# Kernel tuning notes

Hardware: AMD Instinct MI355X
Metric: run time of the kernel (lower is better)

## Reference

```python
import jax, jax.numpy as jnp
import numpy as np

B, L, H, Z = 16, 2048, 1024, 512
NEG = -1e9


def setup_inputs() -> dict:
    key = jax.random.key(0)
    ks = jax.random.split(key, 7)
    return {
        "encoder_rnn_hidden_states": jax.random.normal(ks[0], (B, L, H), jnp.float32),
        "encoder_final_hidden_state": jax.random.normal(ks[1], (B, H), jnp.float32),
        "latent_z_seq": jax.random.normal(ks[2], (B, L, Z), jnp.float32),
        "mask": jax.random.randint(ks[3], (B, L), 0, 2, jnp.int32),
        "weight_q": jax.random.normal(ks[4], (H, H), jnp.float32),
        "weight_k": jax.random.normal(ks[5], (H, H), jnp.float32),
        "weight_v": jax.random.normal(ks[6], (Z, Z), jnp.float32),
    }


def reference(encoder_rnn_hidden_states, encoder_final_hidden_state, latent_z_seq,
              mask, weight_q, weight_k, weight_v):
    temperature = jnp.asarray(weight_q.shape[0] ** 0.5, encoder_rnn_hidden_states.dtype)
    # final hidden state is repeated along src_len, so project once: [B,H]
    k = encoder_final_hidden_state @ weight_k              # [B,H]
    q = encoder_rnn_hidden_states @ weight_q               # [B,L,H]
    v = latent_z_seq @ weight_v                            # [B,L,Z]
    # alignment[b,i,j] = q[b,i] . k[b]  (identical across j, per original repeat)
    alignment = jnp.einsum('bih,bh->bi', q, k) / temperature  # [B,L]
    alignment = jnp.broadcast_to(alignment[:, :, None], (q.shape[0], q.shape[1], q.shape[1]))
    # mask[:, :, None] tiled over last dim; fill -1e9 where mask == 0
    alignment = jnp.where(mask[:, :, None] == 0, NEG, alignment)
    # softmax over the QUERY axis (dim=-2), not the usual key axis
    attn = jax.nn.softmax(alignment, axis=-2)              # [B,L,L]
    output = jnp.einsum('bij,bjz->biz', attn, v)           # [B,L,Z]
    return output, attn
```

## Files before the change

kernel.cpp:

```cpp
#include <hip/hip_runtime.h>

#define BB 16
#define LL 2048
#define HH 1024
#define ZZ 512
#define NEGV -1e9f

__global__ __launch_bounds__(256) void k_proj_k(const float* __restrict__ efhs,
                                                const float* __restrict__ Wk,
                                                float* __restrict__ kbuf) {
    int blk = blockIdx.x;
    int b   = blk >> 5;
    int hpc = (blk >> 3) & 3;
    int hc  = blk & 7;
    int hp  = hpc * 256 + threadIdx.x;
    const float* e  = efhs + b * HH + hc * 128;
    const float* wk = Wk + (size_t)(hc * 128) * HH + hp;
    float acc = 0.f;
#pragma unroll 4
    for (int h = 0; h < 128; ++h)
        acc += e[h] * wk[(size_t)h * HH];
    atomicAdd(&kbuf[b * HH + hp], acc);
}

__global__ __launch_bounds__(256) void k_proj_kq(const float* __restrict__ Wq,
                                                 const float* __restrict__ kbuf,
                                                 float* __restrict__ kq) {
    int h = blockIdx.x >> 2;
    int b = ((blockIdx.x & 3) << 2) + (threadIdx.x >> 6);
    int lane = threadIdx.x & 63;
    const float4* wrow = (const float4*)(Wq + (size_t)h * HH);
    const float4* kb   = (const float4*)(kbuf + b * HH);
    float acc = 0.f;
#pragma unroll
    for (int u = 0; u < 4; ++u) {
        float4 wv = wrow[u * 64 + lane];
        float4 kv = kb[u * 64 + lane];
        acc += wv.x * kv.x + wv.y * kv.y + wv.z * kv.z + wv.w * kv.w;
    }
    for (int off = 32; off > 0; off >>= 1) acc += __shfl_down(acc, off);
    if (lane == 0) kq[b * HH + h] = acc;
}

__global__ __launch_bounds__(256) void k_scores_zsum(const float* __restrict__ erhs,
                                                     const float* __restrict__ kq,
                                                     const int* __restrict__ mask,
                                                     const float* __restrict__ zseq,
                                                     float* __restrict__ sbuf,
                                                     float* __restrict__ zsum) {
    if (blockIdx.x < 8192) {
        int row = blockIdx.x * 4 + (threadIdx.x >> 6);
        int lane = threadIdx.x & 63;
        int b = row >> 11;
        const float4* e  = (const float4*)(erhs + (size_t)row * HH);
        const float4* kb = (const float4*)(kq + b * HH);
        float acc = 0.f;
#pragma unroll
        for (int u = 0; u < 4; ++u) {
            float4 ev = e[u * 64 + lane];
            float4 kv = kb[u * 64 + lane];
            acc += ev.x * kv.x + ev.y * kv.y + ev.z * kv.z + ev.w * kv.w;
        }
        for (int off = 32; off > 0; off >>= 1) acc += __shfl_down(acc, off);
        if (lane == 0) {
            float v = acc * (1.0f / 32.0f);
            if (mask[row] == 0) v = NEGV;
            sbuf[row] = v;
        }
    } else {
        int blk = blockIdx.x - 8192;
        int b = blk >> 5, jc = blk & 31;
        int t = threadIdx.x;
        const float* p = zseq + ((size_t)(b * LL + jc * 64)) * ZZ;
        float a0 = 0.f, a1 = 0.f;
        for (int j = 0; j < 64; ++j) {
            const float* pj = p + (size_t)j * ZZ;
            a0 += pj[t];
            a1 += pj[t + 256];
        }
        atomicAdd(&zsum[b * ZZ + t], a0);
        atomicAdd(&zsum[b * ZZ + t + 256], a1);
    }
}

__global__ __launch_bounds__(256) void k_softmax_vsum(const float* __restrict__ sbuf,
                                                      const float* __restrict__ zsum,
                                                      const float* __restrict__ Wv,
                                                      float* __restrict__ wbuf,
                                                      float* __restrict__ Vs) {
    __shared__ float es[LL];
    __shared__ float red[16];
    if (blockIdx.x < 16) {
        int b = blockIdx.x, tid = threadIdx.x;
        int wave = tid >> 6, lane = tid & 63;
        const float* sb = sbuf + b * LL;
        float m = -3.4e38f;
        for (int i = tid; i < LL; i += 256) m = fmaxf(m, sb[i]);
        for (int off = 32; off > 0; off >>= 1) m = fmaxf(m, __shfl_down(m, off));
        if (lane == 0) red[wave] = m;
        __syncthreads();
        if (tid == 0) {
            float mm = red[0];
            for (int i = 1; i < 4; ++i) mm = fmaxf(mm, red[i]);
            red[0] = mm;
        }
        __syncthreads();
        m = red[0];
        float ssum = 0.f;
        for (int i = tid; i < LL; i += 256) {
            float e = __expf(sb[i] - m);
            es[i] = e;
            ssum += e;
        }
        for (int off = 32; off > 0; off >>= 1) ssum += __shfl_down(ssum, off);
        if (lane == 0) red[8 + wave] = ssum;
        __syncthreads();
        if (tid == 0) {
            float tt = 0.f;
            for (int i = 0; i < 4; ++i) tt += red[8 + i];
            red[8] = tt;
        }
        __syncthreads();
        float inv = 1.0f / red[8];
        for (int i = tid; i < LL; i += 256) wbuf[b * LL + i] = es[i] * inv;
    } else {
        int blk = blockIdx.x - 16;
        int b = blk >> 3, z0c = blk & 7;
        int t = threadIdx.x;
        const float* zs = zsum + b * ZZ + z0c * 64;
        const float* wv = Wv + (size_t)(z0c * 64) * ZZ;
        float a0 = 0.f, a1 = 0.f;
        for (int z0 = 0; z0 < 64; ++z0) {
            float zv = zs[z0];
            const float* wr = wv + (size_t)z0 * ZZ;
            a0 += zv * wr[t];
            a1 += zv * wr[t + 256];
        }
        atomicAdd(&Vs[b * ZZ + t], a0);
        atomicAdd(&Vs[b * ZZ + t + 256], a1);
    }
}

__global__ __launch_bounds__(256) void k_outattn(const float* __restrict__ wbuf,
                                                 const float* __restrict__ Vs,
                                                 float* __restrict__ out,
                                                 float* __restrict__ attn) {
    int row = blockIdx.x;
    int b = row >> 11;
    int t = threadIdx.x;
    float wv = wbuf[row];
    if (t < 128) {
        float4 v = ((const float4*)(Vs + b * ZZ))[t];
        ((float4*)(out + (size_t)row * ZZ))[t] =
            make_float4(wv * v.x, wv * v.y, wv * v.z, wv * v.w);
    }
    float4 pk = make_float4(wv, wv, wv, wv);
    float4* p = (float4*)attn + (size_t)row * 512;
    p[t]       = pk;
    p[t + 256] = pk;
}

extern "C" void kernel_launch(void* const* d_in, const int* in_sizes, int n_in,
                              void* d_out, int out_size, void* d_ws, size_t ws_size,
                              hipStream_t stream) {
    const float* erhs = (const float*)d_in[0];
    const float* efhs = (const float*)d_in[1];
    const float* zseq = (const float*)d_in[2];
    const int*   mask = (const int*)d_in[3];
    const float* Wq   = (const float*)d_in[4];
    const float* Wk   = (const float*)d_in[5];
    const float* Wv   = (const float*)d_in[6];
    float* out = (float*)d_out;

    float* ws   = (float*)d_ws;
    float* zsum = ws;
    float* kbuf = ws + 8192;
    float* Vs   = ws + 24576;
    float* sbuf = ws + 32768;
    float* wbuf = ws + 65536;
    float* kq   = ws + 98304;

    hipMemsetAsync(ws, 0, 32768 * sizeof(float), stream);
    k_proj_k      <<<  512, 256, 0, stream>>>(efhs, Wk, kbuf);
    k_proj_kq     <<< 4096, 256, 0, stream>>>(Wq, kbuf, kq);
    k_scores_zsum <<< 8704, 256, 0, stream>>>(erhs, kq, mask, zseq, sbuf, zsum);
    k_softmax_vsum<<<  144, 256, 0, stream>>>(sbuf, zsum, Wv, wbuf, Vs);
    k_outattn     <<<32768, 256, 0, stream>>>(wbuf, Vs, out,
                                              out + (size_t)BB * LL * ZZ);
}
```

Baseline: 503.4 us.

## Fuse all stages into one cooperative persistent kernel with grid syncs

Replaces the five separate launches with a single cooperative kernel of 1024 blocks that runs every stage (k projection, z sum, kq projection, V sum, scores, softmax, output/attn writes) separated by grid-wide syncs. It also reworks the per-stage work split so each block or wave handles several rows, which reuses loaded k/W vectors across rows and batches. The aim is to remove launch gaps and tail effects between small kernels. In exchange, a grid sync costs something, the softmax stage keeps only 16 blocks busy while the rest wait, and the final write stage uses fewer, larger blocks, which may lower write throughput.

```diff
diff --git a/kernel.cpp b/kernel.cpp
--- a/kernel.cpp
+++ b/kernel.cpp
@@ -1,76 +1,61 @@
 #include <hip/hip_runtime.h>
+#include <hip/hip_cooperative_groups.h>
+
+namespace cg = cooperative_groups;
 
 #define BB 16
 #define LL 2048
 #define HH 1024
 #define ZZ 512
 #define NEGV -1e9f
+#define GRID 1024
 
-__global__ __launch_bounds__(256) void k_proj_k(const float* __restrict__ efhs,
-                                                const float* __restrict__ Wk,
-                                                float* __restrict__ kbuf) {
-    int blk = blockIdx.x;
-    int b   = blk >> 5;
-    int hpc = (blk >> 3) & 3;
-    int hc  = blk & 7;
-    int hp  = hpc * 256 + threadIdx.x;
-    const float* e  = efhs + b * HH + hc * 128;
-    const float* wk = Wk + (size_t)(hc * 128) * HH + hp;
-    float acc = 0.f;
-#pragma unroll 4
-    for (int h = 0; h < 128; ++h)
-        acc += e[h] * wk[(size_t)h * HH];
-    atomicAdd(&kbuf[b * HH + hp], acc);
+__device__ __forceinline__ float dot4(float4 a, float4 b) {
+    return a.x * b.x + a.y * b.y + a.z * b.z + a.w * b.w;
 }
 
-__global__ __launch_bounds__(256) void k_proj_kq(const float* __restrict__ Wq,
-                                                 const float* __restrict__ kbuf,
-                                                 float* __restrict__ kq) {
-    int h = blockIdx.x >> 2;
-    int b = ((blockIdx.x & 3) << 2) + (threadIdx.x >> 6);
-    int lane = threadIdx.x & 63;
-    const float4* wrow = (const float4*)(Wq + (size_t)h * HH);
-    const float4* kb   = (const float4*)(kbuf + b * HH);
-    float acc = 0.f;
-#pragma unroll
-    for (int u = 0; u < 4; ++u) {
-        float4 wv = wrow[u * 64 + lane];
-        float4 kv = kb[u * 64 + lane];
-        acc += wv.x * kv.x + wv.y * kv.y + wv.z * kv.z + wv.w * kv.w;
-    }
-    for (int off = 32; off > 0; off >>= 1) acc += __shfl_down(acc, off);
-    if (lane == 0) kq[b * HH + h] = acc;
-}
+__global__ __launch_bounds__(256, 4) void k_fused(
+    const float* __restrict__ erhs, const float* __restrict__ efhs,
+    const float* __restrict__ zseq, const int* __restrict__ mask,
+    const float* __restrict__ Wq, const float* __restrict__ Wk,
+    const float* __restrict__ Wv, float* __restrict__ out,
+    float* __restrict__ attn, float* __restrict__ ws)
+{
+    float* zsum = ws;
+    float* kbuf = ws + 8192;
+    float* Vs   = ws + 24576;
+    float* sbuf = ws + 32768;
+    float* wbuf = ws + 65536;
+    float* kq   = ws + 98304;
 
-__global__ __launch_bounds__(256) void k_scores_zsum(const float* __restrict__ erhs,
-                                                     const float* __restrict__ kq,
-                                                     const int* __restrict__ mask,
-                                                     const float* __restrict__ zseq,
-                                                     float* __restrict__ sbuf,
-                                                     float* __restrict__ zsum) {
-    if (blockIdx.x < 8192) {
-        int row = blockIdx.x * 4 + (threadIdx.x >> 6);
-        int lane = threadIdx.x & 63;
-        int b = row >> 11;
-        const float4* e  = (const float4*)(erhs + (size_t)row * HH);
-        const float4* kb = (const float4*)(kq + b * HH);
-        float acc = 0.f;
-#pragma unroll
-        for (int u = 0; u < 4; ++u) {
-            float4 ev = e[u * 64 + lane];
-            float4 kv = kb[u * 64 + lane];
-            acc += ev.x * kv.x + ev.y * kv.y + ev.z * kv.z + ev.w * kv.w;
+    cg::grid_group grid = cg::this_grid();
+    const int beta = blockIdx.x;
+    const int t    = threadIdx.x;
+    const int wid  = t >> 6, lane = t & 63;
+
+    __shared__ float es[LL];
+    __shared__ float red[16];
+
+    if (beta < 64) {
+        int b = beta >> 2, hseg = beta & 3;
+        const float* e  = efhs + b * HH + hseg * 256;
+        const float* wk = Wk + (size_t)(hseg * 256) * HH;
+        float a0 = 0.f, a1 = 0.f, a2 = 0.f, a3 = 0.f;
+        for (int h = 0; h < 256; ++h) {
+            float ev = e[h];
+            const float* wr = wk + (size_t)h * HH;
+            a0 += ev * wr[t];
+            a1 += ev * wr[t + 256];
+            a2 += ev * wr[t + 512];
+            a3 += ev * wr[t + 768];
         }
-        for (int off = 32; off > 0; off >>= 1) acc += __shfl_down(acc, off);
-        if (lane == 0) {
-            float v = acc * (1.0f / 32.0f);
-            if (mask[row] == 0) v = NEGV;
-            sbuf[row] = v;
-        }
-    } else {
-        int blk = blockIdx.x - 8192;
+        atomicAdd(&kbuf[b * HH + t],       a0);
+        atomicAdd(&kbuf[b * HH + t + 256], a1);
+        atomicAdd(&kbuf[b * HH + t + 512], a2);
+        atomicAdd(&kbuf[b * HH + t + 768], a3);
+    } else if (beta < 576) {
+        int blk = beta - 64;
         int b = blk >> 5, jc = blk & 31;
-        int t = threadIdx.x;
         const float* p = zseq + ((size_t)(b * LL + jc * 64)) * ZZ;
         float a0 = 0.f, a1 = 0.f;
         for (int j = 0; j < 64; ++j) {
@@ -78,55 +63,26 @@
             a0 += pj[t];
             a1 += pj[t + 256];
         }
-        atomicAdd(&zsum[b * ZZ + t], a0);
+        atomicAdd(&zsum[b * ZZ + t],       a0);
         atomicAdd(&zsum[b * ZZ + t + 256], a1);
     }
-}
+    grid.sync();
 
-__global__ __launch_bounds__(256) void k_softmax_vsum(const float* __restrict__ sbuf,
-                                                      const float* __restrict__ zsum,
-                                                      const float* __restrict__ Wv,
-                                                      float* __restrict__ wbuf,
-                                                      float* __restrict__ Vs) {
-    __shared__ float es[LL];
-    __shared__ float red[16];
-    if (blockIdx.x < 16) {
-        int b = blockIdx.x, tid = threadIdx.x;
-        int wave = tid >> 6, lane = tid & 63;
-        const float* sb = sbuf + b * LL;
-        float m = -3.4e38f;
-        for (int i = tid; i < LL; i += 256) m = fmaxf(m, sb[i]);
-        for (int off = 32; off > 0; off >>= 1) m = fmaxf(m, __shfl_down(m, off));
-        if (lane == 0) red[wave] = m;
-        __syncthreads();
-        if (tid == 0) {
-            float mm = red[0];
-            for (int i = 1; i < 4; ++i) mm = fmaxf(mm, red[i]);
-            red[0] = mm;
+    if (beta < 256) {
+        int h = beta * 4 + wid;
+        const float4* wrow = (const float4*)(Wq + (size_t)h * HH);
+        float4 w0 = wrow[lane], w1 = wrow[64 + lane],
+               w2 = wrow[128 + lane], w3 = wrow[192 + lane];
+        for (int b = 0; b < BB; ++b) {
+            const float4* kb = (const float4*)(kbuf + b * HH);
+            float acc = dot4(w0, kb[lane]) + dot4(w1, kb[64 + lane])
+                      + dot4(w2, kb[128 + lane]) + dot4(w3, kb[192 + lane]);
+            for (int off = 32; off > 0; off >>= 1) acc += __shfl_down(acc, off);
+            if (lane == 0) kq[b * HH + h] = acc;
         }
-        __syncthreads();
-        m = red[0];
-        float ssum = 0.f;
-        for (int i = tid; i < LL; i += 256) {
-            float e = __expf(sb[i] - m);
-            es[i] = e;
-            ssum += e;
-        }
-        for (int off = 32; off > 0; off >>= 1) ssum += __shfl_down(ssum, off);
-        if (lane == 0) red[8 + wave] = ssum;
-        __syncthreads();
-        if (tid == 0) {
-            float tt = 0.f;
-            for (int i = 0; i < 4; ++i) tt += red[8 + i];
-            red[8] = tt;
-        }
-        __syncthreads();
-        float inv = 1.0f / red[8];
-        for (int i = tid; i < LL; i += 256) wbuf[b * LL + i] = es[i] * inv;
-    } else {
-        int blk = blockIdx.x - 16;
+    } else if (beta < 384) {
+        int blk = beta - 256;
         int b = blk >> 3, z0c = blk & 7;
-        int t = threadIdx.x;
         const float* zs = zsum + b * ZZ + z0c * 64;
         const float* wv = Wv + (size_t)(z0c * 64) * ZZ;
         float a0 = 0.f, a1 = 0.f;
@@ -136,28 +92,85 @@
             a0 += zv * wr[t];
             a1 += zv * wr[t + 256];
         }
-        atomicAdd(&Vs[b * ZZ + t], a0);
+        atomicAdd(&Vs[b * ZZ + t],       a0);
         atomicAdd(&Vs[b * ZZ + t + 256], a1);
     }
-}
+    grid.sync();
 
-__global__ __launch_bounds__(256) void k_outattn(const float* __restrict__ wbuf,
-                                                 const float* __restrict__ Vs,
-                                                 float* __restrict__ out,
-                                                 float* __restrict__ attn) {
-    int row = blockIdx.x;
-    int b = row >> 11;
-    int t = threadIdx.x;
-    float wv = wbuf[row];
-    if (t < 128) {
-        float4 v = ((const float4*)(Vs + b * ZZ))[t];
-        ((float4*)(out + (size_t)row * ZZ))[t] =
-            make_float4(wv * v.x, wv * v.y, wv * v.z, wv * v.w);
+    {
+        int gw = beta * 4 + wid;
+        int row0 = gw * 8;
+        int b = row0 >> 11;
+        const float4* kb = (const float4*)(kq + b * HH);
+        float4 k0 = kb[lane], k1 = kb[64 + lane],
+               k2 = kb[128 + lane], k3 = kb[192 + lane];
+        for (int r = 0; r < 8; ++r) {
+            int row = row0 + r;
+            const float4* e = (const float4*)(erhs + (size_t)row * HH);
+            float acc = dot4(e[lane], k0) + dot4(e[64 + lane], k1)
+                      + dot4(e[128 + lane], k2) + dot4(e[192 + lane], k3);
+            for (int off = 32; off > 0; off >>= 1) acc += __shfl_down(acc, off);
+            if (lane == 0) {
+                float v = acc * (1.0f / 32.0f);
+                if (mask[row] == 0) v = NEGV;
+                sbuf[row] = v;
+            }
+        }
     }
-    float4 pk = make_float4(wv, wv, wv, wv);
-    float4* p = (float4*)attn + (size_t)row * 512;
-    p[t]       = pk;
-    p[t + 256] = pk;
+    grid.sync();
+
+    if (beta < 16) {
+        int b = beta;
+        const float* sb = sbuf + b * LL;
+        float m = -3.4e38f;
+        for (int i = t; i < LL; i += 256) m = fmaxf(m, sb[i]);
+        for (int off = 32; off > 0; off >>= 1) m = fmaxf(m, __shfl_down(m, off));
+        if (lane == 0) red[wid] = m;
+        __syncthreads();
+        if (t == 0) {
+            float mm = red[0];
+            for (int i = 1; i < 4; ++i) mm = fmaxf(mm, red[i]);
+            red[0] = mm;
+        }
+        __syncthreads();
+        m = red[0];
+        float ssum = 0.f;
+        for (int i = t; i < LL; i += 256) {
+            float e = __expf(sb[i] - m);
+            es[i] = e;
+            ssum += e;
+        }
+        for (int off = 32; off > 0; off >>= 1) ssum += __shfl_down(ssum, off);
+        if (lane == 0) red[8 + wid] = ssum;
+        __syncthreads();
+        if (t == 0) {
+            float tt = 0.f;
+            for (int i = 0; i < 4; ++i) tt += red[8 + i];
+            red[8] = tt;
+        }
+        __syncthreads();
+        float inv = 1.0f / red[8];
+        for (int i = t; i < LL; i += 256) wbuf[b * LL + i] = es[i] * inv;
+    }
+    grid.sync();
+
+    {
+        int row0 = beta * 32;
+        for (int r = 0; r < 32; ++r) {
+            int row = row0 + r;
+            int b = row >> 11;
+            float wvv = wbuf[row];
+            if (t < 128) {
+                float4 v = ((const float4*)(Vs + b * ZZ))[t];
+                ((float4*)(out + (size_t)row * ZZ))[t] =
+                    make_float4(wvv * v.x, wvv * v.y, wvv * v.z, wvv * v.w);
+            }
+            float4 pk = make_float4(wvv, wvv, wvv, wvv);
+            float4* p = (float4*)attn + (size_t)row * 512;
+            p[t]       = pk;
+            p[t + 256] = pk;
+        }
+    }
 }
 
 extern "C" void kernel_launch(void* const* d_in, const int* in_sizes, int n_in,
@@ -170,21 +183,17 @@
     const float* Wq   = (const float*)d_in[4];
     const float* Wk   = (const float*)d_in[5];
     const float* Wv   = (const float*)d_in[6];
-    float* out = (float*)d_out;
-
+    float* out  = (float*)d_out;
+    float* attn = out + (size_t)BB * LL * ZZ;
     float* ws   = (float*)d_ws;
-    float* zsum = ws;
-    float* kbuf = ws + 8192;
-    float* Vs   = ws + 24576;
-    float* sbuf = ws + 32768;
-    float* wbuf = ws + 65536;
-    float* kq   = ws + 98304;
 
     hipMemsetAsync(ws, 0, 32768 * sizeof(float), stream);
-    k_proj_k      <<<  512, 256, 0, stream>>>(efhs, Wk, kbuf);
-    k_proj_kq     <<< 4096, 256, 0, stream>>>(Wq, kbuf, kq);
-    k_scores_zsum <<< 8704, 256, 0, stream>>>(erhs, kq, mask, zseq, sbuf, zsum);
-    k_softmax_vsum<<<  144, 256, 0, stream>>>(sbuf, zsum, Wv, wbuf, Vs);
-    k_outattn     <<<32768, 256, 0, stream>>>(wbuf, Vs, out,
-                                              out + (size_t)BB * LL * ZZ);
+
+    void* args[] = {
+        (void*)&erhs, (void*)&efhs, (void*)&zseq, (void*)&mask,
+        (void*)&Wq, (void*)&Wk, (void*)&Wv,
+        (void*)&out, (void*)&attn, (void*)&ws,
+    };
+    hipLaunchCooperativeKernel((const void*)k_fused, dim3(GRID), dim3(256),
+                               args, 0, stream);
 }
```

Result: slower. 974.6 us (+93.6%).
